# Performance work log

Measured on AMD Instinct MI355X. Metric: run time of the kernel, lower is better.

## Reference

```python
import jax, jax.numpy as jnp
import numpy as np

B, N, D, H, S = 64, 1000, 512, 8, 20
DK = D // H
TANH_CLIP = 10.0
NEG = -1e9


def setup_inputs() -> dict:
    key = jax.random.key(0)
    k1, k2, k3, k4, k5 = jax.random.split(key, 5)
    embeddings = jax.random.normal(k1, (B, N, D), dtype=jnp.float32)
    q = jax.random.normal(k2, (B, S, D), dtype=jnp.float32)
    # action_mask: True = feasible. Ensure at least one feasible node per row.
    action_mask = jax.random.bernoulli(k3, 0.5, (B, S, N))
    action_mask = action_mask.at[:, :, 0].set(True)
    W_kvl = jax.random.normal(k4, (D, 3 * D), dtype=jnp.float32) * (1.0 / np.sqrt(D))
    W_out = jax.random.normal(k5, (D, D), dtype=jnp.float32) * (1.0 / np.sqrt(D))
    return {"embeddings": embeddings, "q": q, "action_mask": action_mask,
            "W_kvl": W_kvl, "W_out": W_out}


def reference(embeddings, q, action_mask, W_kvl, W_out):
    # _precompute: project node embeddings into glimpse K, V and logit K
    kvl = jnp.einsum('bnd,de->bne', embeddings, W_kvl)  # [B,N,3D]
    glimpse_k, glimpse_v, logit_k = jnp.split(kvl, 3, axis=-1)
    # dynamic embedding is zero (StaticEmbedding for TSP)

    mask = ~action_mask  # True = infeasible, shape [B,S,N]

    # multi-head glimpse attention
    qh = q.reshape(B, S, H, DK)
    kh = glimpse_k.reshape(B, N, H, DK)
    vh = glimpse_v.reshape(B, N, H, DK)
    compat = jnp.einsum('bshd,bnhd->bhsn', qh, kh) / np.sqrt(DK)
    compat = jnp.where(mask[:, None, :, :], NEG, compat)
    attn = jax.nn.softmax(compat, axis=-1)
    heads = jnp.einsum('bhsn,bnhd->bshd', attn, vh).reshape(B, S, D)
    glimpse = jnp.einsum('bsd,de->bse', heads, W_out)  # [B,S,D]

    # pointer logits against logit_k, tanh clipping, mask, log-softmax
    logits = jnp.einsum('bsd,bnd->bsn', glimpse, logit_k) / np.sqrt(D)
    logits = TANH_CLIP * jnp.tanh(logits)
    logits = jnp.where(mask, NEG, logits)
    log_p = jax.nn.log_softmax(logits, axis=-1)  # [B,S,N]

    # rearrange 'b s l -> (s b) l'
    return jnp.swapaxes(log_p, 0, 1).reshape(S * B, N)
```

## Files before the change

### kernel.cpp

```cpp
#include <hip/hip_runtime.h>

#define BB 64
#define NN 1000
#define NP 1024
#define DD 512
#define HH 8
#define SS 20
#define NEGV -1e9f

typedef float v4f __attribute__((ext_vector_type(4)));
typedef short v8s __attribute__((ext_vector_type(8)));
typedef int   v8i __attribute__((ext_vector_type(8)));
typedef int   v4i __attribute__((ext_vector_type(4)));
typedef unsigned char uchar;
typedef unsigned long long ulong_t;

static __device__ __forceinline__ short f2bf(float f) {
    unsigned u = __builtin_bit_cast(unsigned, f);
    u = (u + 0x7fffu + ((u >> 16) & 1u)) >> 16;
    return (short)u;
}
static __device__ __forceinline__ float bf2f(short s) {
    unsigned u = ((unsigned)(unsigned short)s) << 16;
    return __builtin_bit_cast(float, u);
}
static __device__ __forceinline__ uchar f2fp8(float f) {
    return (uchar)(__builtin_amdgcn_cvt_pk_fp8_f32(f, 0.f, 0, false) & 0xff);
}

static __device__ __forceinline__ void gld16(const void* g, void* l) {
    __builtin_amdgcn_global_load_lds(
        (const __attribute__((address_space(1))) void*)(g),
        (__attribute__((address_space(3))) void*)(l),
        16, 0, 0);
}

__global__ void prep(const float* __restrict__ Wkvl, uchar* __restrict__ Wt8,
                     const float* __restrict__ Wout, short* __restrict__ Wot,
                     const float* __restrict__ emb, int* __restrict__ emb8) {
    __shared__ float t[32][33];
    int bid = blockIdx.x, tid = threadIdx.x;
    if (bid < 768) {
        int c0 = (bid % 48) * 32, r0 = (bid / 48) * 32;
        int x = tid & 31, y = tid >> 5;
        for (int k = 0; k < 32; k += 8)
            t[y + k][x] = Wkvl[(long)(r0 + y + k) * 1536 + c0 + x];
        __syncthreads();
        for (int k = 0; k < 32; k += 8)
            Wt8[(long)(c0 + y + k) * 512 + r0 + x] = f2fp8(t[x][y + k]);
    } else if (bid < 1024) {
        int bb = bid - 768;
        int c0 = (bb & 15) * 32, r0 = (bb >> 4) * 32;
        int x = tid & 31, y = tid >> 5;
        for (int k = 0; k < 32; k += 8)
            t[y + k][x] = Wout[(long)(r0 + y + k) * 512 + c0 + x];
        __syncthreads();
        for (int k = 0; k < 32; k += 8)
            Wot[(long)(c0 + y + k) * 512 + r0 + x] = f2bf(t[x][y + k]);
    } else {
        int i = (bid - 1024) * 256 + tid;
        long o = (long)i * 8;
        v4f a = *(const v4f*)(emb + o);
        v4f b = *(const v4f*)(emb + o + 4);
        int lo = __builtin_amdgcn_cvt_pk_fp8_f32(a.x, a.y, 0, false);
        lo = __builtin_amdgcn_cvt_pk_fp8_f32(a.z, a.w, lo, true);
        int hi = __builtin_amdgcn_cvt_pk_fp8_f32(b.x, b.y, 0, false);
        hi = __builtin_amdgcn_cvt_pk_fp8_f32(b.z, b.w, hi, true);
        int2 r; r.x = lo; r.y = hi;
        *(int2*)(emb8 + i * 2) = r;
    }
}

__global__ __launch_bounds__(512, 2) void gemm_kvl(const uchar* __restrict__ emb8,
                                                   const uchar* __restrict__ Wt8,
                                                   uchar* __restrict__ kvl8) {
    extern __shared__ __align__(16) uchar smem[];
    uchar* As0 = smem;
    uchar* Bs0 = smem + 65536;
    int tid = threadIdx.x;
    int id = blockIdx.x;
    int xcd = id & 7, j0 = id >> 3;
    int wgid = (xcd < 4 ? xcd * 188 : 752 + (xcd - 4) * 187) + j0;
    int m_idx = wgid / 6, n_idx = wgid - m_idx * 6;
    int m0 = m_idx * 256, n0 = n_idx * 256;
    int wid = tid >> 6, lane = tid & 63, quad = lane >> 4, l16 = lane & 15;
    int wm = wid & 1, wn = wid >> 1;
    const uchar* Ag = emb8 + (long)m0 * 512;
    const uchar* Bg = Wt8 + (long)n0 * 512;
    int rsub = lane >> 3;
    int kc = ((lane & 7) ^ rsub) * 16;

    v4f acc[8][4] = {};

    auto stageA = [&](int bi, int kk) {
        #pragma unroll
        for (int p = 0; p < 4; ++p) {
            int rl = wid * 32 + p * 8;
            gld16(Ag + (long)(rl + rsub) * 512 + kk + kc, As0 + bi * 32768 + rl * 128);
        }
    };
    auto stageB = [&](int bi, int kk) {
        #pragma unroll
        for (int p = 0; p < 4; ++p) {
            int rl = wid * 32 + p * 8;
            gld16(Bg + (long)(rl + rsub) * 512 + kk + kc, Bs0 + bi * 32768 + rl * 128);
        }
    };
    auto ldfrag = [&](const uchar* base, int row) -> v8i {
        int c0 = (quad * 2) ^ (row & 7);
        v4i lo = *(const v4i*)(base + row * 128 + c0 * 16);
        v4i hi = *(const v4i*)(base + row * 128 + (c0 ^ 1) * 16);
        return __builtin_shufflevector(lo, hi, 0, 1, 2, 3, 4, 5, 6, 7);
    };

    stageA(0, 0); stageB(0, 0);
    stageA(1, 128); stageB(1, 128);
    asm volatile("s_waitcnt vmcnt(8)" ::: "memory");
    __builtin_amdgcn_s_barrier();
    __builtin_amdgcn_sched_barrier(0);

    v8i af[4], bf[4];
    #pragma unroll
    for (int t = 0; t < 4; ++t) {
        int cur = t & 1;
        const uchar* ab = As0 + cur * 32768;
        const uchar* bb = Bs0 + cur * 32768;
        int kn2 = (t + 2) * 128;
        #pragma unroll
        for (int i = 0; i < 4; ++i) af[i] = ldfrag(ab, wm * 128 + i * 16 + l16);
        #pragma unroll
        for (int jj = 0; jj < 2; ++jj) bf[jj] = ldfrag(bb, wn * 64 + jj * 16 + l16);
        __builtin_amdgcn_s_barrier();
        __builtin_amdgcn_s_setprio(1);
        #pragma unroll
        for (int i = 0; i < 4; ++i)
            #pragma unroll
            for (int jj = 0; jj < 2; ++jj)
                acc[i][jj] = __builtin_amdgcn_mfma_scale_f32_16x16x128_f8f6f4(
                    af[i], bf[jj], acc[i][jj], 0, 0, 0, 0x7f7f7f7f, 0, 0x7f7f7f7f);
        __builtin_amdgcn_s_setprio(0);
        __builtin_amdgcn_s_barrier();
        #pragma unroll
        for (int jj = 2; jj < 4; ++jj) bf[jj] = ldfrag(bb, wn * 64 + jj * 16 + l16);
        __builtin_amdgcn_s_barrier();
        __builtin_amdgcn_s_setprio(1);
        #pragma unroll
        for (int i = 0; i < 4; ++i)
            #pragma unroll
            for (int jj = 2; jj < 4; ++jj)
                acc[i][jj] = __builtin_amdgcn_mfma_scale_f32_16x16x128_f8f6f4(
                    af[i], bf[jj], acc[i][jj], 0, 0, 0, 0x7f7f7f7f, 0, 0x7f7f7f7f);
        __builtin_amdgcn_s_setprio(0);
        __builtin_amdgcn_s_barrier();
        #pragma unroll
        for (int i = 0; i < 4; ++i) af[i] = ldfrag(ab, wm * 128 + (i + 4) * 16 + l16);
        if (t < 2) stageB(cur, kn2);
        __builtin_amdgcn_s_barrier();
        __builtin_amdgcn_s_setprio(1);
        #pragma unroll
        for (int i = 0; i < 4; ++i)
            #pragma unroll
            for (int jj = 0; jj < 2; ++jj)
                acc[i + 4][jj] = __builtin_amdgcn_mfma_scale_f32_16x16x128_f8f6f4(
                    af[i], bf[jj], acc[i + 4][jj], 0, 0, 0, 0x7f7f7f7f, 0, 0x7f7f7f7f);
        __builtin_amdgcn_s_setprio(0);
        __builtin_amdgcn_s_barrier();
        if (t < 2) stageA(cur, kn2);
        __builtin_amdgcn_s_setprio(1);
        #pragma unroll
        for (int i = 0; i < 4; ++i)
            #pragma unroll
            for (int jj = 2; jj < 4; ++jj)
                acc[i + 4][jj] = __builtin_amdgcn_mfma_scale_f32_16x16x128_f8f6f4(
                    af[i], bf[jj], acc[i + 4][jj], 0, 0, 0, 0x7f7f7f7f, 0, 0x7f7f7f7f);
        __builtin_amdgcn_s_setprio(0);
        if (t < 3) {
            if (t < 2) asm volatile("s_waitcnt vmcnt(8)" ::: "memory");
            else       asm volatile("s_waitcnt vmcnt(0)" ::: "memory");
            __builtin_amdgcn_s_barrier();
            __builtin_amdgcn_sched_barrier(0);
        }
    }
    __syncthreads();

    short* rp = (short*)smem;
    short* r = rp + wid * (16 * 72);
    #pragma unroll
    for (int i = 0; i < 8; ++i) {
        #pragma unroll
        for (int jj = 0; jj < 4; ++jj)
            #pragma unroll
            for (int rr = 0; rr < 4; ++rr)
                r[(quad * 4 + rr) * 72 + jj * 16 + l16] = f2bf(acc[i][jj][rr]);
        #pragma unroll
        for (int h = 0; h < 2; ++h) {
            int rowl = h * 8 + (lane >> 3);
            int colc = (lane & 7) * 8;
            v8s val = *(const v8s*)(r + rowl * 72 + colc);
            int lo = __builtin_amdgcn_cvt_pk_fp8_f32(bf2f(val[0]), bf2f(val[1]), 0, false);
            lo = __builtin_amdgcn_cvt_pk_fp8_f32(bf2f(val[2]), bf2f(val[3]), lo, true);
            int hi = __builtin_amdgcn_cvt_pk_fp8_f32(bf2f(val[4]), bf2f(val[5]), 0, false);
            hi = __builtin_amdgcn_cvt_pk_fp8_f32(bf2f(val[6]), bf2f(val[7]), hi, true);
            int2 st; st.x = lo; st.y = hi;
            *(int2*)(kvl8 + (long)(m0 + wm * 128 + i * 16 + rowl) * 1536 +
                     n0 + wn * 64 + colc) = st;
        }
    }
}

__global__ void transpose_v(const uchar* __restrict__ kvl8, uchar* __restrict__ Vt8) {
    int bh = blockIdx.x, b = bh >> 3, h = bh & 7;
    int n0 = blockIdx.y * 64;
    __shared__ uchar T[64][72];
    int tid = threadIdx.x;
    #pragma unroll
    for (int it = 0; it < 2; ++it) {
        int nl = (tid >> 3) + it * 32;
        int n = n0 + nl;
        int nc = n < NN ? n : NN - 1;
        int d0 = (tid & 7) * 8;
        ulong_t v = *(const ulong_t*)(kvl8 + ((long)b * NN + nc) * 1536 + DD + h * 64 + d0);
        uchar* vb = (uchar*)&v;
        #pragma unroll
        for (int j = 0; j < 8; ++j) T[d0 + j][nl] = vb[j];
    }
    __syncthreads();
    #pragma unroll
    for (int it = 0; it < 2; ++it) {
        int d = (tid >> 3) + it * 32;
        int ns = (tid & 7) * 8;
        *(ulong_t*)(Vt8 + ((long)bh * 64 + d) * NP + n0 + ns) = *(const ulong_t*)&T[d][ns];
    }
}

#define CST 1036
__global__ __launch_bounds__(512) void attn_fused(const float* __restrict__ q,
                                                  const uchar* __restrict__ kvl8,
                                                  const uchar* __restrict__ Vt8,
                                                  const int* __restrict__ mask,
                                                  float* __restrict__ heads) {
    int b = blockIdx.x, h = blockIdx.y;
    __shared__ __align__(16) uchar qs[32 * 72];
    __shared__ __align__(16) short cmp[SS * CST];
    int tid = threadIdx.x, wid = tid >> 6, lane = tid & 63, quad = lane >> 4, l16 = lane & 15;
    for (int i = tid; i < 32 * 64; i += 512) {
        int row = i >> 6, col = i & 63;
        float v = (row < SS) ? q[((long)b * SS + row) * DD + h * 64 + col] : 0.f;
        qs[row * 72 + col] = f2fp8(v);
    }
    __syncthreads();
    long af[2][2];
    #pragma unroll
    for (int mt = 0; mt < 2; ++mt)
        #pragma unroll
        for (int ks = 0; ks < 2; ++ks)
            af[mt][ks] = *(const long*)(qs + (mt * 16 + l16) * 72 + ks * 32 + quad * 8);
    for (int t = 0; t < 8; ++t) {
        int nt = wid * 8 + t;
        int n = nt * 16 + l16;
        int nc = n < NN ? n : NN - 1;
        const uchar* kp = kvl8 + ((long)b * NN + nc) * 1536 + h * 64 + quad * 8;
        long b0 = *(const long*)kp;
        long b1 = *(const long*)(kp + 32);
        #pragma unroll
        for (int mt = 0; mt < 2; ++mt) {
            v4f a = {};
            a = __builtin_amdgcn_mfma_f32_16x16x32_fp8_fp8(af[mt][0], b0, a, 0, 0, 0);
            a = __builtin_amdgcn_mfma_f32_16x16x32_fp8_fp8(af[mt][1], b1, a, 0, 0, 0);
            #pragma unroll
            for (int r = 0; r < 4; ++r) {
                int s = mt * 16 + quad * 4 + r;
                if (s < SS) cmp[s * CST + nt * 16 + l16] = f2bf(a[r] * 0.125f);
            }
        }
    }
    __syncthreads();
    for (int s = wid; s < SS; s += 8) {
        const int* mr = mask + ((long)b * SS + s) * NN;
        float x[16];
        float mx = NEGV;
        #pragma unroll
        for (int i = 0; i < 16; ++i) {
            int n = lane + 64 * i;
            float v = bf2f(cmp[s * CST + n]);
            bool feas = (n < NN) && (mr[n < NN ? n : 0] != 0);
            x[i] = feas ? v : NEGV;
            mx = fmaxf(mx, x[i]);
        }
        for (int off = 32; off; off >>= 1) mx = fmaxf(mx, __shfl_xor(mx, off));
        float sum = 0.f;
        #pragma unroll
        for (int i = 0; i < 16; ++i) { x[i] = __expf(x[i] - mx); sum += x[i]; }
        for (int off = 32; off; off >>= 1) sum += __shfl_xor(sum, off);
        float inv = 1.0f / sum;
        uchar* pr = (uchar*)cmp + (long)s * (CST * 2);
        #pragma unroll
        for (int i = 0; i < 16; ++i) pr[lane + 64 * i] = f2fp8(x[i] * inv);
    }
    __syncthreads();
    int mt = wid & 1, dt = wid >> 1;
    int srow = mt * 16 + l16; if (srow > SS - 1) srow = SS - 1;
    const uchar* ap = (const uchar*)cmp + (long)srow * (CST * 2) + quad * 8;
    const uchar* vb = Vt8 + (long)(b * HH + h) * 64 * NP;
    v4f acc = {};
    for (int k0 = 0; k0 < NP; k0 += 32) {
        long afr = *(const long*)(ap + k0);
        long bfr = *(const long*)(vb + (long)(dt * 16 + l16) * NP + k0 + quad * 8);
        acc = __builtin_amdgcn_mfma_f32_16x16x32_fp8_fp8(afr, bfr, acc, 0, 0, 0);
    }
    #pragma unroll
    for (int r = 0; r < 4; ++r) {
        int s = mt * 16 + quad * 4 + r;
        if (s < SS)
            heads[((long)b * SS + s) * DD + h * 64 + dt * 16 + l16] = acc[r];
    }
}

__global__ __launch_bounds__(256) void out_proj(const float* __restrict__ heads,
                                                const short* __restrict__ Wot,
                                                float* __restrict__ glimpse) {
    __shared__ __align__(16) short As[64 * 40], Bs[64 * 40];
    int tid = threadIdx.x;
    int m0 = blockIdx.x * 64, n0 = blockIdx.y * 64;
    int wid = tid >> 6, lane = tid & 63, quad = lane >> 4, l16 = lane & 15;
    int wm = wid & 1, wn = wid >> 1;
    int arow = tid >> 3, akol = (tid & 7) * 4;
    int brow = tid >> 2, bkol = (tid & 3) * 8;
    v4f acc[2][2] = {};
    for (int kk = 0; kk < 512; kk += 32) {
        #pragma unroll
        for (int p = 0; p < 2; ++p) {
            int r = arow + p * 32;
            v4f a = *(const v4f*)(heads + (long)(m0 + r) * 512 + kk + akol);
            short4 s4;
            s4.x = f2bf(a.x); s4.y = f2bf(a.y); s4.z = f2bf(a.z); s4.w = f2bf(a.w);
            *(short4*)(As + r * 40 + akol) = s4;
        }
        *(uint4*)(Bs + brow * 40 + bkol) =
            *(const uint4*)(Wot + (long)(n0 + brow) * 512 + kk + bkol);
        __syncthreads();
        #pragma unroll
        for (int i = 0; i < 2; ++i) {
            v8s af = *(const v8s*)(As + (wm * 32 + i * 16 + l16) * 40 + quad * 8);
            #pragma unroll
            for (int j = 0; j < 2; ++j) {
                v8s bf = *(const v8s*)(Bs + (wn * 32 + j * 16 + l16) * 40 + quad * 8);
                acc[i][j] = __builtin_amdgcn_mfma_f32_16x16x32_bf16(af, bf, acc[i][j], 0, 0, 0);
            }
        }
        __syncthreads();
    }
    #pragma unroll
    for (int i = 0; i < 2; ++i)
        #pragma unroll
        for (int j = 0; j < 2; ++j)
            #pragma unroll
            for (int r = 0; r < 4; ++r)
                glimpse[(long)(m0 + wm * 32 + i * 16 + quad * 4 + r) * 512 +
                        n0 + wn * 32 + j * 16 + l16] = acc[i][j][r];
}

__global__ __launch_bounds__(256) void ptr_logits(const float* __restrict__ glimpse,
                                                  const uchar* __restrict__ kvl8,
                                                  float* __restrict__ logits) {
    int b = blockIdx.x, g = blockIdx.y;
    __shared__ __align__(16) uchar Gs[32 * 520];
    int tid = threadIdx.x;
    #pragma unroll
    for (int it = 0; it < 16; ++it) {
        int e = it * 1024 + tid * 4;
        int row = e >> 9, col = e & 511;
        int pk = 0;
        if (row < SS) {
            v4f a = *(const v4f*)(glimpse + ((long)b * SS + row) * 512 + col);
            pk = __builtin_amdgcn_cvt_pk_fp8_f32(a.x, a.y, 0, false);
            pk = __builtin_amdgcn_cvt_pk_fp8_f32(a.z, a.w, pk, true);
        }
        *(int*)(Gs + row * 520 + col) = pk;
    }
    __syncthreads();
    int wid = tid >> 6, lane = tid & 63, quad = lane >> 4, l16 = lane & 15;
    const float scale = 0.04419417382415922f;
    int nt = g * 4 + wid;
    int n = nt * 16 + l16;
    int ncl = n < NN ? n : NN - 1;
    const uchar* kp = kvl8 + ((long)b * NN + ncl) * 1536 + 1024 + quad * 8;
    v4f acc[2] = {};
    for (int k = 0; k < 16; ++k) {
        long bfr = *(const long*)(kp + k * 32);
        #pragma unroll
        for (int m = 0; m < 2; ++m) {
            long afr = *(const long*)(Gs + (m * 16 + l16) * 520 + k * 32 + quad * 8);
            acc[m] = __builtin_amdgcn_mfma_f32_16x16x32_fp8_fp8(afr, bfr, acc[m], 0, 0, 0);
        }
    }
    #pragma unroll
    for (int m = 0; m < 2; ++m)
        #pragma unroll
        for (int r = 0; r < 4; ++r) {
            int s = m * 16 + quad * 4 + r;
            if (s < SS)
                logits[((long)b * SS + s) * NP + nt * 16 + l16] = acc[m][r] * scale;
        }
}

__global__ __launch_bounds__(256) void logsoftmax_out(const float* __restrict__ logits,
                                                      const int* __restrict__ mask,
                                                      float* __restrict__ out) {
    int row = blockIdx.x;
    int b = row / SS, s = row % SS;
    int tid = threadIdx.x;
    __shared__ float red[8];
    int n0 = tid * 4;
    v4f v = *(const v4f*)(logits + (long)row * NP + n0);
    const int* mr = mask + (long)row * NN;
    float x[4];
    float mx = NEGV;
    #pragma unroll
    for (int j = 0; j < 4; ++j) {
        int n = n0 + j;
        float t = 10.f * tanhf(v[j]);
        bool feas = (n < NN) && (mr[n < NN ? n : 0] != 0);
        x[j] = feas ? t : NEGV;
        mx = fmaxf(mx, x[j]);
    }
    for (int off = 32; off; off >>= 1) mx = fmaxf(mx, __shfl_xor(mx, off));
    int wid = tid >> 6, lane = tid & 63;
    if (lane == 0) red[wid] = mx;
    __syncthreads();
    mx = fmaxf(fmaxf(red[0], red[1]), fmaxf(red[2], red[3]));
    float sum = 0.f;
    #pragma unroll
    for (int j = 0; j < 4; ++j) sum += __expf(x[j] - mx);
    for (int off = 32; off; off >>= 1) sum += __shfl_xor(sum, off);
    __syncthreads();
    if (lane == 0) red[4 + wid] = sum;
    __syncthreads();
    sum = red[4] + red[5] + red[6] + red[7];
    float lse = mx + __logf(sum);
    float* orow = out + ((long)s * BB + b) * NN;
    #pragma unroll
    for (int j = 0; j < 4; ++j) {
        int n = n0 + j;
        if (n < NN) orow[n] = x[j] - lse;
    }
}

extern "C" void kernel_launch(void* const* d_in, const int* in_sizes, int n_in,
                              void* d_out, int out_size, void* d_ws, size_t ws_size,
                              hipStream_t stream) {
    const float* emb  = (const float*)d_in[0];
    const float* q    = (const float*)d_in[1];
    const int*   mask = (const int*)d_in[2];
    const float* Wkvl = (const float*)d_in[3];
    const float* Wout = (const float*)d_in[4];
    float* out = (float*)d_out;

    char* ws = (char*)d_ws;
    uchar* kvl8    = (uchar*)ws; ws += (size_t)64000 * 1536;
    uchar* Vt8     = (uchar*)ws; ws += (size_t)512 * 64 * NP;
    uchar* Wt8     = (uchar*)ws; ws += (size_t)1536 * 512;
    uchar* emb8    = (uchar*)ws; ws += (size_t)64000 * 512;
    short* Wot     = (short*)ws; ws += (size_t)512 * 512 * 2;
    float* heads   = (float*)ws; ws += (size_t)BB * SS * DD * 4;
    float* glimpse = (float*)ws; ws += (size_t)BB * SS * DD * 4;
    float* logits  = (float*)ws; ws += (size_t)BB * SS * NP * 4;

    static int s_attr_done = 0;
    if (!s_attr_done) {
        hipFuncSetAttribute(reinterpret_cast<const void*>(gemm_kvl),
                            hipFuncAttributeMaxDynamicSharedMemorySize, 131072);
        s_attr_done = 1;
    }

    prep<<<dim3(1024 + 16000), 256, 0, stream>>>(Wkvl, Wt8, Wout, Wot, emb, (int*)emb8);
    gemm_kvl<<<dim3(1500), 512, 131072, stream>>>(emb8, Wt8, kvl8);
    transpose_v<<<dim3(512, 16), 256, 0, stream>>>(kvl8, Vt8);
    attn_fused<<<dim3(BB, HH), 512, 0, stream>>>(q, kvl8, Vt8, mask, heads);
    out_proj<<<dim3(20, 8), 256, 0, stream>>>(heads, Wot, glimpse);
    ptr_logits<<<dim3(BB, 16), 256, 0, stream>>>(glimpse, kvl8, logits);
    logsoftmax_out<<<dim3(BB * SS), 256, 0, stream>>>(logits, mask, out);
}
```

Baseline: 346.4 us.

## Software-pipeline LDS fragment loads across MFMA quadrants and swizzle epilogue staging

Restructures the FP8 projection GEMM main loop so that A/B fragments for the next quadrant and the next k-tile are loaded from LDS while the current MFMAs run, using double fragment registers. Most intra-iteration barriers are removed, and global staging is interleaved with different wait counts. The epilogue's bf16 staging buffer switches from a padded layout to an XOR-swizzled 128-byte row layout to avoid bank conflicts. This raises register pressure and relies on a subtler barrier and waitcnt ordering for correctness.

```diff
diff --git a/kernel.cpp b/kernel.cpp
--- a/kernel.cpp
+++ b/kernel.cpp
@@ -113,97 +113,103 @@
         return __builtin_shufflevector(lo, hi, 0, 1, 2, 3, 4, 5, 6, 7);
     };
 
+    v8i afA[4], afB[4], bfA[2], bfB[2];
+
     stageA(0, 0); stageB(0, 0);
     stageA(1, 128); stageB(1, 128);
     asm volatile("s_waitcnt vmcnt(8)" ::: "memory");
     __builtin_amdgcn_s_barrier();
-    __builtin_amdgcn_sched_barrier(0);
-
-    v8i af[4], bf[4];
+    #pragma unroll
+    for (int i = 0; i < 4; ++i) afA[i] = ldfrag(As0, wm * 128 + i * 16 + l16);
+    #pragma unroll
+    for (int j = 0; j < 2; ++j) bfA[j] = ldfrag(Bs0, wn * 64 + j * 16 + l16);
+
     #pragma unroll
     for (int t = 0; t < 4; ++t) {
-        int cur = t & 1;
-        const uchar* ab = As0 + cur * 32768;
-        const uchar* bb = Bs0 + cur * 32768;
+        const uchar* ab  = As0 + (t & 1) * 32768;
+        const uchar* bb  = Bs0 + (t & 1) * 32768;
+        const uchar* abn = As0 + ((t & 1) ^ 1) * 32768;
+        const uchar* bbn = Bs0 + ((t & 1) ^ 1) * 32768;
         int kn2 = (t + 2) * 128;
         #pragma unroll
-        for (int i = 0; i < 4; ++i) af[i] = ldfrag(ab, wm * 128 + i * 16 + l16);
-        #pragma unroll
-        for (int jj = 0; jj < 2; ++jj) bf[jj] = ldfrag(bb, wn * 64 + jj * 16 + l16);
-        __builtin_amdgcn_s_barrier();
+        for (int j = 0; j < 2; ++j) bfB[j] = ldfrag(bb, wn * 64 + (j + 2) * 16 + l16);
         __builtin_amdgcn_s_setprio(1);
         #pragma unroll
         for (int i = 0; i < 4; ++i)
             #pragma unroll
-            for (int jj = 0; jj < 2; ++jj)
-                acc[i][jj] = __builtin_amdgcn_mfma_scale_f32_16x16x128_f8f6f4(
-                    af[i], bf[jj], acc[i][jj], 0, 0, 0, 0x7f7f7f7f, 0, 0x7f7f7f7f);
+            for (int j = 0; j < 2; ++j)
+                acc[i][j] = __builtin_amdgcn_mfma_scale_f32_16x16x128_f8f6f4(
+                    afA[i], bfA[j], acc[i][j], 0, 0, 0, 0x7f7f7f7f, 0, 0x7f7f7f7f);
         __builtin_amdgcn_s_setprio(0);
-        __builtin_amdgcn_s_barrier();
-        #pragma unroll
-        for (int jj = 2; jj < 4; ++jj) bf[jj] = ldfrag(bb, wn * 64 + jj * 16 + l16);
-        __builtin_amdgcn_s_barrier();
+        #pragma unroll
+        for (int i = 0; i < 4; ++i) afB[i] = ldfrag(ab, wm * 128 + (i + 4) * 16 + l16);
         __builtin_amdgcn_s_setprio(1);
         #pragma unroll
         for (int i = 0; i < 4; ++i)
             #pragma unroll
-            for (int jj = 2; jj < 4; ++jj)
-                acc[i][jj] = __builtin_amdgcn_mfma_scale_f32_16x16x128_f8f6f4(
-                    af[i], bf[jj], acc[i][jj], 0, 0, 0, 0x7f7f7f7f, 0, 0x7f7f7f7f);
+            for (int j = 0; j < 2; ++j)
+                acc[i][j + 2] = __builtin_amdgcn_mfma_scale_f32_16x16x128_f8f6f4(
+                    afA[i], bfB[j], acc[i][j + 2], 0, 0, 0, 0x7f7f7f7f, 0, 0x7f7f7f7f);
         __builtin_amdgcn_s_setprio(0);
-        __builtin_amdgcn_s_barrier();
-        #pragma unroll
-        for (int i = 0; i < 4; ++i) af[i] = ldfrag(ab, wm * 128 + (i + 4) * 16 + l16);
-        if (t < 2) stageB(cur, kn2);
-        __builtin_amdgcn_s_barrier();
+        if (t < 2) {
+            __builtin_amdgcn_s_barrier();
+            stageB(t & 1, kn2);
+        }
         __builtin_amdgcn_s_setprio(1);
         #pragma unroll
         for (int i = 0; i < 4; ++i)
             #pragma unroll
-            for (int jj = 0; jj < 2; ++jj)
-                acc[i + 4][jj] = __builtin_amdgcn_mfma_scale_f32_16x16x128_f8f6f4(
-                    af[i], bf[jj], acc[i + 4][jj], 0, 0, 0, 0x7f7f7f7f, 0, 0x7f7f7f7f);
-        __builtin_amdgcn_s_setprio(0);
-        __builtin_amdgcn_s_barrier();
-        if (t < 2) stageA(cur, kn2);
-        __builtin_amdgcn_s_setprio(1);
-        #pragma unroll
-        for (int i = 0; i < 4; ++i)
-            #pragma unroll
-            for (int jj = 2; jj < 4; ++jj)
-                acc[i + 4][jj] = __builtin_amdgcn_mfma_scale_f32_16x16x128_f8f6f4(
-                    af[i], bf[jj], acc[i + 4][jj], 0, 0, 0, 0x7f7f7f7f, 0, 0x7f7f7f7f);
+            for (int j = 0; j < 2; ++j)
+                acc[i + 4][j] = __builtin_amdgcn_mfma_scale_f32_16x16x128_f8f6f4(
+                    afB[i], bfA[j], acc[i + 4][j], 0, 0, 0, 0x7f7f7f7f, 0, 0x7f7f7f7f);
         __builtin_amdgcn_s_setprio(0);
         if (t < 3) {
-            if (t < 2) asm volatile("s_waitcnt vmcnt(8)" ::: "memory");
+            if (t < 2) asm volatile("s_waitcnt vmcnt(4)" ::: "memory");
             else       asm volatile("s_waitcnt vmcnt(0)" ::: "memory");
             __builtin_amdgcn_s_barrier();
-            __builtin_amdgcn_sched_barrier(0);
-        }
-    }
-    __syncthreads();
-
-    short* rp = (short*)smem;
-    short* r = rp + wid * (16 * 72);
+            #pragma unroll
+            for (int i = 0; i < 4; ++i) afA[i] = ldfrag(abn, wm * 128 + i * 16 + l16);
+            #pragma unroll
+            for (int j = 0; j < 2; ++j) bfA[j] = ldfrag(bbn, wn * 64 + j * 16 + l16);
+            if (t < 2) stageA(t & 1, kn2);
+        }
+        __builtin_amdgcn_s_setprio(1);
+        #pragma unroll
+        for (int i = 0; i < 4; ++i)
+            #pragma unroll
+            for (int j = 0; j < 2; ++j)
+                acc[i + 4][j + 2] = __builtin_amdgcn_mfma_scale_f32_16x16x128_f8f6f4(
+                    afB[i], bfB[j], acc[i + 4][j + 2], 0, 0, 0, 0x7f7f7f7f, 0, 0x7f7f7f7f);
+        __builtin_amdgcn_s_setprio(0);
+    }
+    __syncthreads();
+
+    uchar* rbase = smem + wid * 2048;
     #pragma unroll
     for (int i = 0; i < 8; ++i) {
         #pragma unroll
         for (int jj = 0; jj < 4; ++jj)
             #pragma unroll
-            for (int rr = 0; rr < 4; ++rr)
-                r[(quad * 4 + rr) * 72 + jj * 16 + l16] = f2bf(acc[i][jj][rr]);
+            for (int rr = 0; rr < 4; ++rr) {
+                int row = quad * 4 + rr;
+                int col = jj * 16 + l16;
+                int chunk = (col >> 3) ^ ((row >> 1) & 7);
+                *(short*)(rbase + row * 128 + chunk * 16 + (col & 7) * 2) =
+                    f2bf(acc[i][jj][rr]);
+            }
         #pragma unroll
         for (int h = 0; h < 2; ++h) {
             int rowl = h * 8 + (lane >> 3);
-            int colc = (lane & 7) * 8;
-            v8s val = *(const v8s*)(r + rowl * 72 + colc);
+            int cc = lane & 7;
+            int chunk = cc ^ ((rowl >> 1) & 7);
+            v8s val = *(const v8s*)(rbase + rowl * 128 + chunk * 16);
             int lo = __builtin_amdgcn_cvt_pk_fp8_f32(bf2f(val[0]), bf2f(val[1]), 0, false);
             lo = __builtin_amdgcn_cvt_pk_fp8_f32(bf2f(val[2]), bf2f(val[3]), lo, true);
             int hi = __builtin_amdgcn_cvt_pk_fp8_f32(bf2f(val[4]), bf2f(val[5]), 0, false);
             hi = __builtin_amdgcn_cvt_pk_fp8_f32(bf2f(val[6]), bf2f(val[7]), hi, true);
             int2 st; st.x = lo; st.y = hi;
             *(int2*)(kvl8 + (long)(m0 + wm * 128 + i * 16 + rowl) * 1536 +
-                     n0 + wn * 64 + colc) = st;
+                     n0 + wn * 64 + cc * 8) = st;
         }
     }
 }
```

After: 424.1 us. 22.4% more time.

## Shrink KVL GEMM tile to 128x128 with 4 waves and simpler pipeline

Applied to the files above, without the earlier changes.

The FP8 projection GEMM moves from 256x256 tiles with 8 waves to 128x128 tiles with 4 waves, launching 6000 workgroups with 64 KB of LDS each. The K-loop drops the interleaved A/B staging and extra barriers and stages A and B together after the first MFMA half. The XCD-aware workgroup remap is simplified to match. Smaller tiles raise the number of resident blocks and shrink the tail, but each tile gets less reuse, so global and LDS traffic per FLOP goes up.

```diff
diff --git a/kernel.cpp b/kernel.cpp
--- a/kernel.cpp
+++ b/kernel.cpp
@@ -71,18 +71,17 @@
     }
 }
 
-__global__ __launch_bounds__(512, 2) void gemm_kvl(const uchar* __restrict__ emb8,
-                                                   const uchar* __restrict__ Wt8,
-                                                   uchar* __restrict__ kvl8) {
+__global__ __launch_bounds__(256) void gemm_kvl(const uchar* __restrict__ emb8,
+                                                const uchar* __restrict__ Wt8,
+                                                uchar* __restrict__ kvl8) {
     extern __shared__ __align__(16) uchar smem[];
     uchar* As0 = smem;
-    uchar* Bs0 = smem + 65536;
+    uchar* Bs0 = smem + 32768;
     int tid = threadIdx.x;
     int id = blockIdx.x;
-    int xcd = id & 7, j0 = id >> 3;
-    int wgid = (xcd < 4 ? xcd * 188 : 752 + (xcd - 4) * 187) + j0;
-    int m_idx = wgid / 6, n_idx = wgid - m_idx * 6;
-    int m0 = m_idx * 256, n0 = n_idx * 256;
+    int wgid = (id & 7) * 750 + (id >> 3);
+    int m_idx = wgid / 12, n_idx = wgid - m_idx * 12;
+    int m0 = m_idx * 128, n0 = n_idx * 128;
     int wid = tid >> 6, lane = tid & 63, quad = lane >> 4, l16 = lane & 15;
     int wm = wid & 1, wn = wid >> 1;
     const uchar* Ag = emb8 + (long)m0 * 512;
@@ -90,20 +89,18 @@
     int rsub = lane >> 3;
     int kc = ((lane & 7) ^ rsub) * 16;
 
-    v4f acc[8][4] = {};
-
-    auto stageA = [&](int bi, int kk) {
+    v4f acc[4][4] = {};
+
+    auto stageAB = [&](int bi, int kk) {
         #pragma unroll
         for (int p = 0; p < 4; ++p) {
             int rl = wid * 32 + p * 8;
-            gld16(Ag + (long)(rl + rsub) * 512 + kk + kc, As0 + bi * 32768 + rl * 128);
-        }
-    };
-    auto stageB = [&](int bi, int kk) {
+            gld16(Ag + (long)(rl + rsub) * 512 + kk + kc, As0 + bi * 16384 + rl * 128);
+        }
         #pragma unroll
         for (int p = 0; p < 4; ++p) {
             int rl = wid * 32 + p * 8;
-            gld16(Bg + (long)(rl + rsub) * 512 + kk + kc, Bs0 + bi * 32768 + rl * 128);
+            gld16(Bg + (long)(rl + rsub) * 512 + kk + kc, Bs0 + bi * 16384 + rl * 128);
         }
     };
     auto ldfrag = [&](const uchar* base, int row) -> v8i {
@@ -113,8 +110,8 @@
         return __builtin_shufflevector(lo, hi, 0, 1, 2, 3, 4, 5, 6, 7);
     };
 
-    stageA(0, 0); stageB(0, 0);
-    stageA(1, 128); stageB(1, 128);
+    stageAB(0, 0);
+    stageAB(1, 128);
     asm volatile("s_waitcnt vmcnt(8)" ::: "memory");
     __builtin_amdgcn_s_barrier();
     __builtin_amdgcn_sched_barrier(0);
@@ -123,56 +120,30 @@
     #pragma unroll
     for (int t = 0; t < 4; ++t) {
         int cur = t & 1;
-        const uchar* ab = As0 + cur * 32768;
-        const uchar* bb = Bs0 + cur * 32768;
-        int kn2 = (t + 2) * 128;
-        #pragma unroll
-        for (int i = 0; i < 4; ++i) af[i] = ldfrag(ab, wm * 128 + i * 16 + l16);
-        #pragma unroll
-        for (int jj = 0; jj < 2; ++jj) bf[jj] = ldfrag(bb, wn * 64 + jj * 16 + l16);
+        const uchar* ab = As0 + cur * 16384;
+        const uchar* bb = Bs0 + cur * 16384;
+        #pragma unroll
+        for (int i = 0; i < 4; ++i) af[i] = ldfrag(ab, wm * 64 + i * 16 + l16);
+        #pragma unroll
+        for (int j = 0; j < 4; ++j) bf[j] = ldfrag(bb, wn * 64 + j * 16 + l16);
+        __builtin_amdgcn_s_setprio(1);
+        #pragma unroll
+        for (int i = 0; i < 4; ++i)
+            #pragma unroll
+            for (int j = 0; j < 2; ++j)
+                acc[i][j] = __builtin_amdgcn_mfma_scale_f32_16x16x128_f8f6f4(
+                    af[i], bf[j], acc[i][j], 0, 0, 0, 0x7f7f7f7f, 0, 0x7f7f7f7f);
+        __builtin_amdgcn_s_setprio(0);
+        asm volatile("s_waitcnt lgkmcnt(0)" ::: "memory");
         __builtin_amdgcn_s_barrier();
+        if (t < 2) stageAB(cur, (t + 2) * 128);
         __builtin_amdgcn_s_setprio(1);
         #pragma unroll
         for (int i = 0; i < 4; ++i)
             #pragma unroll
-            for (int jj = 0; jj < 2; ++jj)
-                acc[i][jj] = __builtin_amdgcn_mfma_scale_f32_16x16x128_f8f6f4(
-                    af[i], bf[jj], acc[i][jj], 0, 0, 0, 0x7f7f7f7f, 0, 0x7f7f7f7f);
-        __builtin_amdgcn_s_setprio(0);
-        __builtin_amdgcn_s_barrier();
-        #pragma unroll
-        for (int jj = 2; jj < 4; ++jj) bf[jj] = ldfrag(bb, wn * 64 + jj * 16 + l16);
-        __builtin_amdgcn_s_barrier();
-        __builtin_amdgcn_s_setprio(1);
-        #pragma unroll
-        for (int i = 0; i < 4; ++i)
-            #pragma unroll
-            for (int jj = 2; jj < 4; ++jj)
-                acc[i][jj] = __builtin_amdgcn_mfma_scale_f32_16x16x128_f8f6f4(
-                    af[i], bf[jj], acc[i][jj], 0, 0, 0, 0x7f7f7f7f, 0, 0x7f7f7f7f);
-        __builtin_amdgcn_s_setprio(0);
-        __builtin_amdgcn_s_barrier();
-        #pragma unroll
-        for (int i = 0; i < 4; ++i) af[i] = ldfrag(ab, wm * 128 + (i + 4) * 16 + l16);
-        if (t < 2) stageB(cur, kn2);
-        __builtin_amdgcn_s_barrier();
-        __builtin_amdgcn_s_setprio(1);
-        #pragma unroll
-        for (int i = 0; i < 4; ++i)
-            #pragma unroll
-            for (int jj = 0; jj < 2; ++jj)
-                acc[i + 4][jj] = __builtin_amdgcn_mfma_scale_f32_16x16x128_f8f6f4(
-                    af[i], bf[jj], acc[i + 4][jj], 0, 0, 0, 0x7f7f7f7f, 0, 0x7f7f7f7f);
-        __builtin_amdgcn_s_setprio(0);
-        __builtin_amdgcn_s_barrier();
-        if (t < 2) stageA(cur, kn2);
-        __builtin_amdgcn_s_setprio(1);
-        #pragma unroll
-        for (int i = 0; i < 4; ++i)
-            #pragma unroll
-            for (int jj = 2; jj < 4; ++jj)
-                acc[i + 4][jj] = __builtin_amdgcn_mfma_scale_f32_16x16x128_f8f6f4(
-                    af[i], bf[jj], acc[i + 4][jj], 0, 0, 0, 0x7f7f7f7f, 0, 0x7f7f7f7f);
+            for (int j = 2; j < 4; ++j)
+                acc[i][j] = __builtin_amdgcn_mfma_scale_f32_16x16x128_f8f6f4(
+                    af[i], bf[j], acc[i][j], 0, 0, 0, 0x7f7f7f7f, 0, 0x7f7f7f7f);
         __builtin_amdgcn_s_setprio(0);
         if (t < 3) {
             if (t < 2) asm volatile("s_waitcnt vmcnt(8)" ::: "memory");
@@ -186,7 +157,7 @@
     short* rp = (short*)smem;
     short* r = rp + wid * (16 * 72);
     #pragma unroll
-    for (int i = 0; i < 8; ++i) {
+    for (int i = 0; i < 4; ++i) {
         #pragma unroll
         for (int jj = 0; jj < 4; ++jj)
             #pragma unroll
@@ -202,7 +173,7 @@
             int hi = __builtin_amdgcn_cvt_pk_fp8_f32(bf2f(val[4]), bf2f(val[5]), 0, false);
             hi = __builtin_amdgcn_cvt_pk_fp8_f32(bf2f(val[6]), bf2f(val[7]), hi, true);
             int2 st; st.x = lo; st.y = hi;
-            *(int2*)(kvl8 + (long)(m0 + wm * 128 + i * 16 + rowl) * 1536 +
+            *(int2*)(kvl8 + (long)(m0 + wm * 64 + i * 16 + rowl) * 1536 +
                      n0 + wn * 64 + colc) = st;
         }
     }
@@ -469,12 +440,12 @@
     static int s_attr_done = 0;
     if (!s_attr_done) {
         hipFuncSetAttribute(reinterpret_cast<const void*>(gemm_kvl),
-                            hipFuncAttributeMaxDynamicSharedMemorySize, 131072);
+                            hipFuncAttributeMaxDynamicSharedMemorySize, 65536);
         s_attr_done = 1;
     }
 
     prep<<<dim3(1024 + 16000), 256, 0, stream>>>(Wkvl, Wt8, Wout, Wot, emb, (int*)emb8);
-    gemm_kvl<<<dim3(1500), 512, 131072, stream>>>(emb8, Wt8, kvl8);
+    gemm_kvl<<<dim3(6000), 256, 65536, stream>>>(emb8, Wt8, kvl8);
     transpose_v<<<dim3(512, 16), 256, 0, stream>>>(kvl8, Vt8);
     attn_fused<<<dim3(BB, HH), 512, 0, stream>>>(q, kvl8, Vt8, mask, heads);
     out_proj<<<dim3(20, 8), 256, 0, stream>>>(heads, Wot, glimpse);
```

Result: no change. 349.2 us (+0.8%).
